# Kernel tuning notes

Measured on AMD Instinct MI355X. Metric: run time of the kernel, lower is better.

## Reference

```python
import jax, jax.numpy as jnp
import numpy as np

N_NODES = 10000
N_EDGES = 160000
D = 512            # input_dim = hidden_size = output_dim
NUM_EXPERTS = 4
N_LAYERS = 2


def setup_inputs() -> dict:
    key = jax.random.key(0)
    k = jax.random.split(key, 7)
    x = jax.random.normal(k[0], (N_NODES, D), dtype=jnp.float32)
    edge_index = jax.random.randint(k[1], (2, N_EDGES), 0, N_NODES, dtype=jnp.int32)
    # Gating network (Linear D -> NUM_EXPERTS)
    gate_w = jax.random.normal(k[2], (D, NUM_EXPERTS), dtype=jnp.float32) * 0.05
    gate_b = jnp.zeros((NUM_EXPERTS,), dtype=jnp.float32)
    # Per-expert SAGEConv weights: lin_r (self/root) and lin_l (neighbor) + bias
    w_self = jax.random.normal(k[3], (NUM_EXPERTS, N_LAYERS, D, D), dtype=jnp.float32) * 0.05
    w_neigh = jax.random.normal(k[4], (NUM_EXPERTS, N_LAYERS, D, D), dtype=jnp.float32) * 0.05
    b_exp = jnp.zeros((NUM_EXPERTS, N_LAYERS, D), dtype=jnp.float32)
    return {"x": x, "edge_index": edge_index, "gate_w": gate_w, "gate_b": gate_b,
            "w_self": w_self, "w_neigh": w_neigh, "b_exp": b_exp, "top_k": 1}


def reference(x, edge_index, gate_w, gate_b, w_self, w_neigh, b_exp, top_k):
    n = x.shape[0]
    src, dst = edge_index[0], edge_index[1]
    # mean-aggregation normalization (PyG SAGEConv aggr='mean'); 0 for isolated nodes
    deg = jax.ops.segment_sum(jnp.ones_like(src, dtype=x.dtype), dst, num_segments=n)
    inv_deg = jnp.where(deg > 0, 1.0 / jnp.maximum(deg, 1.0), 0.0)[:, None]  # [N,1]

    # gating: softmax(Linear(x)) then top-k routing
    gate = jax.nn.softmax(x @ gate_w + gate_b, axis=-1)          # [N, E]
    top_vals, top_idx = jax.lax.top_k(gate, top_k)               # [N, k]

    def expert(ws, wn, b):  # ws, wn: [L, D, D]; b: [L, D]
        h = x
        for l in range(N_LAYERS):
            agg = jax.ops.segment_sum(h[src], dst, num_segments=n) * inv_deg
            # SAGEConv: lin_l(mean_neigh) + lin_r(x) + bias, then relu (norm='id', eval dropout)
            h = jax.nn.relu(agg @ wn[l] + h @ ws[l] + b[l])
        return h

    # dense all-expert compute (matches original module)
    outs = jax.vmap(expert)(w_self, w_neigh, b_exp)              # [E, N, D]
    outs = jnp.transpose(outs, (1, 0, 2))                        # [N, E, D]
    sel = jnp.take_along_axis(outs, top_idx[:, :, None], axis=1)  # [N, k, D]
    return jnp.sum(sel * top_vals[:, :, None], axis=1)           # [N, D]
```

## Files before the change

kernel.cpp:

```cpp
#include <hip/hip_runtime.h>
#include <hip/hip_bf16.h>
#include <cstdint>

#define N_NODES 10000
#define N_EDGES 160000
#define DIM 512
#define K1 1024
#define NEXP 4

typedef __bf16 bf16_t;
typedef bf16_t bf16x8 __attribute__((ext_vector_type(8)));
typedef float f32x4 __attribute__((ext_vector_type(4)));

#define AS1(p) ((__attribute__((address_space(1))) void*)(p))
#define AS3(p) ((__attribute__((address_space(3))) void*)(p))

__global__ void zero_kernel(int* __restrict__ deg, int* __restrict__ ecnt) {
    int i = blockIdx.x * blockDim.x + threadIdx.x;
    if (i < N_NODES) deg[i] = 0;
    if (i < NEXP) ecnt[i] = 0;
}

__global__ void gate_kernel(const float* __restrict__ x,
                            const float* __restrict__ gw,
                            const float* __restrict__ gb,
                            int* __restrict__ top_idx,
                            float* __restrict__ top_val,
                            bf16_t* __restrict__ acat) {
    const int wave = threadIdx.x >> 6;
    const int lane = threadIdx.x & 63;
    const int node = blockIdx.x * 4 + wave;
    if (node >= N_NODES) return;
    const float4* x4 = (const float4*)(x + (size_t)node * DIM);
    const float4* gw4 = (const float4*)gw;
    float4 xa = x4[lane * 2];
    float4 xb = x4[lane * 2 + 1];
    float xv[8] = { xa.x, xa.y, xa.z, xa.w, xb.x, xb.y, xb.z, xb.w };
    float a0 = 0.f, a1 = 0.f, a2 = 0.f, a3 = 0.f;
    #pragma unroll
    for (int c = 0; c < 8; c++) {
        float4 g = gw4[lane * 8 + c];
        a0 += xv[c] * g.x; a1 += xv[c] * g.y; a2 += xv[c] * g.z; a3 += xv[c] * g.w;
    }
    bf16x8 o;
    #pragma unroll
    for (int c = 0; c < 8; c++) o[c] = (bf16_t)xv[c];
    *(bf16x8*)(acat + (size_t)node * K1 + DIM + lane * 8) = o;
    for (int off = 32; off > 0; off >>= 1) {
        a0 += __shfl_xor(a0, off);
        a1 += __shfl_xor(a1, off);
        a2 += __shfl_xor(a2, off);
        a3 += __shfl_xor(a3, off);
    }
    if (lane == 0) {
        float z[4] = { a0 + gb[0], a1 + gb[1], a2 + gb[2], a3 + gb[3] };
        int bi = 0; float bm = z[0];
        for (int e = 1; e < 4; e++) if (z[e] > bm) { bm = z[e]; bi = e; }
        float den = 0.f;
        for (int e = 0; e < 4; e++) den += expf(z[e] - bm);
        top_idx[node] = bi;
        top_val[node] = 1.0f / den;
    }
}

__global__ void bucket_kernel(const int* __restrict__ top_idx,
                              int* __restrict__ ecnt,
                              int* __restrict__ lists) {
    __shared__ int lcnt[NEXP];
    __shared__ int base[NEXP];
    const int tid = threadIdx.x;
    if (tid < NEXP) lcnt[tid] = 0;
    __syncthreads();
    const int node = blockIdx.x * 256 + tid;
    int e = 0, rank = 0;
    if (node < N_NODES) {
        e = top_idx[node];
        rank = atomicAdd(&lcnt[e], 1);
    }
    __syncthreads();
    if (tid < NEXP) base[tid] = atomicAdd(&ecnt[tid], lcnt[tid]);
    __syncthreads();
    if (node < N_NODES) lists[e * N_NODES + base[e] + rank] = node;
}

__global__ void deg_kernel(const int* __restrict__ dst, int* __restrict__ deg) {
    int i = blockIdx.x * blockDim.x + threadIdx.x;
    if (i < N_EDGES) atomicAdd(&deg[dst[i]], 1);
}

__global__ void scan_kernel(const int* __restrict__ deg,
                            int* __restrict__ offs,
                            int* __restrict__ cursor) {
    __shared__ int wsum[16];
    __shared__ int carrysh;
    const int tid = threadIdx.x;
    const int lane = tid & 63;
    const int wv = tid >> 6;
    if (tid == 0) carrysh = 0;
    __syncthreads();
    for (int base = 0; base < N_NODES; base += 1024) {
        int i = base + tid;
        int v = (i < N_NODES) ? deg[i] : 0;
        int s = v;
        #pragma unroll
        for (int off = 1; off < 64; off <<= 1) {
            int t = __shfl_up(s, off);
            if (lane >= off) s += t;
        }
        if (lane == 63) wsum[wv] = s;
        int carry = carrysh;
        __syncthreads();
        if (wv == 0) {
            int w = (lane < 16) ? wsum[lane] : 0;
            #pragma unroll
            for (int off = 1; off < 16; off <<= 1) {
                int t = __shfl_up(w, off);
                if (lane >= off) w += t;
            }
            if (lane < 16) wsum[lane] = w;
        }
        __syncthreads();
        int wbase = (wv > 0) ? wsum[wv - 1] : 0;
        int excl = carry + wbase + s - v;
        if (i < N_NODES) { offs[i] = excl; cursor[i] = excl; }
        int total = wsum[15];
        __syncthreads();
        if (tid == 0) carrysh = carry + total;
        __syncthreads();
    }
    if (tid == 0) offs[N_NODES] = carrysh;
}

__global__ void fill_kernel(const int* __restrict__ src, const int* __restrict__ dst,
                            int* __restrict__ cursor, int* __restrict__ csr) {
    int i = blockIdx.x * blockDim.x + threadIdx.x;
    if (i < N_EDGES) {
        int d = dst[i];
        int p = atomicAdd(&cursor[d], 1);
        csr[p] = src[i];
    }
}

__global__ void wtrans_kernel(const float* __restrict__ w_neigh,
                              const float* __restrict__ w_self,
                              bf16_t* __restrict__ Bt) {
    __shared__ float tile[32][33];
    const int m = blockIdx.z;
    const bool isSelf = m >= 8;
    const int el = m & 7;
    const float* W = (isSelf ? w_self : w_neigh) + (size_t)el * DIM * DIM;
    const int k0 = blockIdx.x * 32;
    const int n0 = blockIdx.y * 32;
    const int tx = threadIdx.x, ty = threadIdx.y;
    for (int r = ty; r < 32; r += 8)
        tile[r][tx] = W[(size_t)(k0 + r) * DIM + n0 + tx];
    __syncthreads();
    for (int r = ty; r < 32; r += 8) {
        int n = n0 + r;
        int k = k0 + tx;
        Bt[((size_t)el * DIM + n) * K1 + (isSelf ? DIM : 0) + k] = (bf16_t)tile[tx][r];
    }
}

__global__ void agg1_kernel(const int* __restrict__ offs, const int* __restrict__ csr,
                            bf16_t* __restrict__ acat) {
    const int wave = threadIdx.x >> 6;
    const int lane = threadIdx.x & 63;
    const int node = blockIdx.x * 4 + wave;
    if (node >= N_NODES) return;
    const int c0 = lane * 8;
    float s[8] = {0,0,0,0,0,0,0,0};
    int beg = offs[node];
    int end = offs[node + 1];
    int d = end - beg;
    int p = beg;
    for (; p + 8 <= end; p += 8) {
        bf16x8 v[8];
        #pragma unroll
        for (int q = 0; q < 8; q++) {
            int idx = csr[p + q];
            v[q] = *(const bf16x8*)(acat + (size_t)idx * K1 + DIM + c0);
        }
        #pragma unroll
        for (int q = 0; q < 8; q++)
            #pragma unroll
            for (int k = 0; k < 8; k++) s[k] += (float)v[q][k];
    }
    for (; p + 4 <= end; p += 4) {
        bf16x8 v[4];
        #pragma unroll
        for (int q = 0; q < 4; q++) {
            int idx = csr[p + q];
            v[q] = *(const bf16x8*)(acat + (size_t)idx * K1 + DIM + c0);
        }
        #pragma unroll
        for (int q = 0; q < 4; q++)
            #pragma unroll
            for (int k = 0; k < 8; k++) s[k] += (float)v[q][k];
    }
    for (; p < end; p++) {
        int idx = csr[p];
        bf16x8 v0 = *(const bf16x8*)(acat + (size_t)idx * K1 + DIM + c0);
        #pragma unroll
        for (int k = 0; k < 8; k++) s[k] += (float)v0[k];
    }
    float w = d > 0 ? 1.0f / (float)d : 0.0f;
    bf16x8 o;
    #pragma unroll
    for (int k = 0; k < 8; k++) o[k] = (bf16_t)(s[k] * w);
    *(bf16x8*)(acat + (size_t)node * K1 + c0) = o;
}

__global__ void agg2_kernel(const int* __restrict__ offs, const int* __restrict__ csr,
                            const int* __restrict__ top_idx,
                            const bf16_t* __restrict__ h1, bf16_t* __restrict__ acat) {
    const int wave = threadIdx.x >> 6;
    const int lane = threadIdx.x & 63;
    const int node = blockIdx.x * 4 + wave;
    if (node >= N_NODES) return;
    const int c0 = lane * 8;
    const bf16_t* hb = h1 + (size_t)top_idx[node] * N_NODES * DIM;
    float s[8] = {0,0,0,0,0,0,0,0};
    int beg = offs[node];
    int end = offs[node + 1];
    int d = end - beg;
    int p = beg;
    for (; p + 8 <= end; p += 8) {
        bf16x8 v[8];
        #pragma unroll
        for (int q = 0; q < 8; q++) {
            int idx = csr[p + q];
            v[q] = *(const bf16x8*)(hb + (size_t)idx * DIM + c0);
        }
        #pragma unroll
        for (int q = 0; q < 8; q++)
            #pragma unroll
            for (int k = 0; k < 8; k++) s[k] += (float)v[q][k];
    }
    for (; p + 4 <= end; p += 4) {
        bf16x8 v[4];
        #pragma unroll
        for (int q = 0; q < 4; q++) {
            int idx = csr[p + q];
            v[q] = *(const bf16x8*)(hb + (size_t)idx * DIM + c0);
        }
        #pragma unroll
        for (int q = 0; q < 4; q++)
            #pragma unroll
            for (int k = 0; k < 8; k++) s[k] += (float)v[q][k];
    }
    for (; p < end; p++) {
        int idx = csr[p];
        bf16x8 v0 = *(const bf16x8*)(hb + (size_t)idx * DIM + c0);
        #pragma unroll
        for (int k = 0; k < 8; k++) s[k] += (float)v0[k];
    }
    float w = d > 0 ? 1.0f / (float)d : 0.0f;
    bf16x8 o;
    #pragma unroll
    for (int k = 0; k < 8; k++) o[k] = (bf16_t)(s[k] * w);
    *(bf16x8*)(acat + (size_t)node * K1 + c0) = o;
    *(bf16x8*)(acat + (size_t)node * K1 + DIM + c0) = *(const bf16x8*)(hb + (size_t)node * DIM + c0);
}

__global__ __launch_bounds__(256)
void gemm1_kernel(const bf16_t* __restrict__ A,
                  const bf16_t* __restrict__ Bt,
                  const float* __restrict__ bias_all,
                  bf16_t* __restrict__ h1) {
    const int b = blockIdx.x;
    const int kq = b & 7;
    const int ke = kq >> 2;
    const int ky = kq & 3;
    const int r = b >> 3;
    const int yloc = r >> 3;
    const int xz = r & 7;
    const int bx = xz & 3;
    const int e = ke * 2 + (xz >> 2);
    const int by = ky * 20 + yloc;
    if (by >= 79) return;

    __shared__ __align__(16) bf16_t As[128 * 32];
    __shared__ __align__(16) bf16_t Bs[128 * 32];

    const int t = threadIdx.x;
    const int lane = t & 63;
    const int wave = t >> 6;
    const int wm = wave >> 1;
    const int wn = wave & 1;

    const int r0 = t >> 2;
    const int rot = (t >> 3) & 3;
    const int cgl = ((t & 3) - rot) & 3;

    int i0 = by * 128 + r0;
    int i1 = i0 + 64;
    int arow0 = min(i0, N_NODES - 1);
    int arow1 = min(i1, N_NODES - 1);

    const bf16_t* Bte = Bt + (size_t)(e * 2) * DIM * K1;
    const bf16_t* aptr0 = A + (size_t)arow0 * K1 + cgl * 8;
    const bf16_t* aptr1 = A + (size_t)arow1 * K1 + cgl * 8;
    const bf16_t* bptr0 = Bte + (size_t)(bx * 128 + r0) * K1 + cgl * 8;
    const bf16_t* bptr1 = bptr0 + (size_t)64 * K1;

    f32x4 acc[4][4] = {};
    char* asb = (char*)&As[0];
    char* bsb = (char*)&Bs[0];
    const int wb = wave * 1024;

    const int cpr = lane >> 4;
    const int rfr = lane & 15;

    for (int k0 = 0; k0 < K1; k0 += 32) {
        __syncthreads();
        __builtin_amdgcn_global_load_lds(AS1(aptr0), AS3(asb + wb),        16, 0, 0);
        __builtin_amdgcn_global_load_lds(AS1(aptr1), AS3(asb + 4096 + wb), 16, 0, 0);
        __builtin_amdgcn_global_load_lds(AS1(bptr0), AS3(bsb + wb),        16, 0, 0);
        __builtin_amdgcn_global_load_lds(AS1(bptr1), AS3(bsb + 4096 + wb), 16, 0, 0);
        __syncthreads();
        bf16x8 af[4], bfr[4];
        #pragma unroll
        for (int i = 0; i < 4; i++) {
            int rf = wm * 64 + i * 16 + rfr;
            int pp = (cpr + (rf >> 1)) & 3;
            af[i] = *(const bf16x8*)(As + rf * 32 + pp * 8);
        }
        #pragma unroll
        for (int j = 0; j < 4; j++) {
            int rf = wn * 64 + j * 16 + rfr;
            int pp = (cpr + (rf >> 1)) & 3;
            bfr[j] = *(const bf16x8*)(Bs + rf * 32 + pp * 8);
        }
        #pragma unroll
        for (int i = 0; i < 4; i++)
            #pragma unroll
            for (int j = 0; j < 4; j++)
                acc[i][j] = __builtin_amdgcn_mfma_f32_16x16x32_bf16(af[i], bfr[j], acc[i][j], 0, 0, 0);
        aptr0 += 32; aptr1 += 32; bptr0 += 32; bptr1 += 32;
    }

    const float* bias = bias_all + e * 1024;
    const int cbase = bx * 128 + wn * 64 + (lane & 15);
    float bv[4];
    #pragma unroll
    for (int j = 0; j < 4; j++) bv[j] = bias[cbase + j * 16];
    #pragma unroll
    for (int i = 0; i < 4; i++) {
        #pragma unroll
        for (int rr = 0; rr < 4; rr++) {
            int row = by * 128 + wm * 64 + i * 16 + (lane >> 4) * 4 + rr;
            if (row < N_NODES) {
                bf16_t* cp = h1 + ((size_t)e * N_NODES + row) * DIM + cbase;
                #pragma unroll
                for (int j = 0; j < 4; j++) {
                    float v = fmaxf(acc[i][j][rr] + bv[j], 0.f);
                    cp[j * 16] = (bf16_t)v;
                }
            }
        }
    }
}

__global__ __launch_bounds__(256)
void gemm2_kernel(const bf16_t* __restrict__ A,
                  const bf16_t* __restrict__ Bt,
                  const float* __restrict__ bias_all,
                  float* __restrict__ out,
                  const int* __restrict__ lists,
                  const int* __restrict__ ecnt,
                  const float* __restrict__ top_val) {
    const int bx = blockIdx.x, by = blockIdx.y, e = blockIdx.z;
    const int cnt = ecnt[e];
    if (by * 64 >= cnt) return;

    __shared__ __align__(16) bf16_t As[64 * 32];
    __shared__ __align__(16) bf16_t Bs[128 * 32];

    const int t = threadIdx.x;
    const int lane = t & 63;
    const int wave = t >> 6;

    const int r0 = t >> 2;
    const int rot = (t >> 3) & 3;
    const int cgl = ((t & 3) - rot) & 3;

    int i0 = by * 64 + r0;
    int arow0 = lists[e * N_NODES + min(i0, cnt - 1)];

    const bf16_t* Bte = Bt + (size_t)(e * 2 + 1) * DIM * K1;
    const bf16_t* aptr0 = A + (size_t)arow0 * K1 + cgl * 8;
    const bf16_t* bptr0 = Bte + (size_t)(bx * 128 + r0) * K1 + cgl * 8;
    const bf16_t* bptr1 = bptr0 + (size_t)64 * K1;

    f32x4 acc[4][2] = {};
    char* asb = (char*)&As[0];
    char* bsb = (char*)&Bs[0];
    const int wb = wave * 1024;

    const int cpr = lane >> 4;
    const int rfr = lane & 15;

    for (int k0 = 0; k0 < K1; k0 += 32) {
        __syncthreads();
        __builtin_amdgcn_global_load_lds(AS1(aptr0), AS3(asb + wb),        16, 0, 0);
        __builtin_amdgcn_global_load_lds(AS1(bptr0), AS3(bsb + wb),        16, 0, 0);
        __builtin_amdgcn_global_load_lds(AS1(bptr1), AS3(bsb + 4096 + wb), 16, 0, 0);
        __syncthreads();
        bf16x8 af[4], bfr[2];
        #pragma unroll
        for (int i = 0; i < 4; i++) {
            int rf = i * 16 + rfr;
            int pp = (cpr + (rf >> 1)) & 3;
            af[i] = *(const bf16x8*)(As + rf * 32 + pp * 8);
        }
        #pragma unroll
        for (int j = 0; j < 2; j++) {
            int rf = wave * 32 + j * 16 + rfr;
            int pp = (cpr + (rf >> 1)) & 3;
            bfr[j] = *(const bf16x8*)(Bs + rf * 32 + pp * 8);
        }
        #pragma unroll
        for (int i = 0; i < 4; i++)
            #pragma unroll
            for (int j = 0; j < 2; j++)
                acc[i][j] = __builtin_amdgcn_mfma_f32_16x16x32_bf16(af[i], bfr[j], acc[i][j], 0, 0, 0);
        aptr0 += 32; bptr0 += 32; bptr1 += 32;
    }

    const float* bias = bias_all + e * 1024 + DIM;
    const int cbase = bx * 128 + wave * 32 + (lane & 15);
    float bv[2];
    #pragma unroll
    for (int j = 0; j < 2; j++) bv[j] = bias[cbase + j * 16];
    #pragma unroll
    for (int i = 0; i < 4; i++) {
        #pragma unroll
        for (int rr = 0; rr < 4; rr++) {
            int row = by * 64 + i * 16 + (lane >> 4) * 4 + rr;
            if (row < cnt) {
                int node = lists[e * N_NODES + row];
                float tv = top_val[node];
                float* cp = out + (size_t)node * DIM + cbase;
                #pragma unroll
                for (int j = 0; j < 2; j++) {
                    float v = fmaxf(acc[i][j][rr] + bv[j], 0.f);
                    cp[j * 16] = v * tv;
                }
            }
        }
    }
}

extern "C" void kernel_launch(void* const* d_in, const int* in_sizes, int n_in,
                              void* d_out, int out_size, void* d_ws, size_t ws_size,
                              hipStream_t stream) {
    const float* x       = (const float*)d_in[0];
    const int*   edge    = (const int*)d_in[1];
    const float* gw      = (const float*)d_in[2];
    const float* gb      = (const float*)d_in[3];
    const float* w_self  = (const float*)d_in[4];
    const float* w_neigh = (const float*)d_in[5];
    const float* b_exp   = (const float*)d_in[6];
    float* out = (float*)d_out;

    char* p = (char*)d_ws;
    auto alloc = [&](size_t bytes) {
        char* r = p;
        p += (bytes + 255) & ~(size_t)255;
        return r;
    };
    bf16_t* Bt      = (bf16_t*)alloc((size_t)8 * DIM * K1 * 2);
    bf16_t* acat    = (bf16_t*)alloc((size_t)N_NODES * K1 * 2);
    bf16_t* h1      = (bf16_t*)alloc((size_t)NEXP * N_NODES * DIM * 2);
    int*    deg     = (int*)alloc((size_t)N_NODES * 4);
    int*    offs    = (int*)alloc((size_t)(N_NODES + 1) * 4);
    int*    cursor  = (int*)alloc((size_t)N_NODES * 4);
    int*    csr     = (int*)alloc((size_t)N_EDGES * 4);
    int*    top_idx = (int*)alloc((size_t)N_NODES * 4);
    float*  top_val = (float*)alloc((size_t)N_NODES * 4);
    int*    ecnt    = (int*)alloc(256);
    int*    lists   = (int*)alloc((size_t)NEXP * N_NODES * 4);

    const int* srcE = edge;
    const int* dstE = edge + N_EDGES;

    zero_kernel<<<40, 256, 0, stream>>>(deg, ecnt);
    gate_kernel<<<N_NODES / 4, 256, 0, stream>>>(x, gw, gb, top_idx, top_val, acat);
    bucket_kernel<<<40, 256, 0, stream>>>(top_idx, ecnt, lists);
    deg_kernel<<<N_EDGES / 256, 256, 0, stream>>>(dstE, deg);
    scan_kernel<<<1, 1024, 0, stream>>>(deg, offs, cursor);
    fill_kernel<<<N_EDGES / 256, 256, 0, stream>>>(srcE, dstE, cursor, csr);
    wtrans_kernel<<<dim3(16, 16, 16), dim3(32, 8), 0, stream>>>(w_neigh, w_self, Bt);
    agg1_kernel<<<N_NODES / 4, 256, 0, stream>>>(offs, csr, acat);
    gemm1_kernel<<<1280, 256, 0, stream>>>(acat, Bt, b_exp, h1);
    agg2_kernel<<<N_NODES / 4, 256, 0, stream>>>(offs, csr, top_idx, h1, acat);
    gemm2_kernel<<<dim3(4, 157, 4), 256, 0, stream>>>(acat, Bt, b_exp, out, lists, ecnt, top_val);
}
```

Before: 281.2 us.

## Double-buffer LDS tiles in both GEMM kernels to overlap loads with MFMA

Both GEMM kernels now keep two LDS buffers for the A and B tiles. The next K-slice is issued with global_load_lds before the MFMAs on the current slice, and each iteration needs one barrier instead of two. The goal is to hide global-to-LDS latency behind matrix compute and cut barrier stalls. In exchange it doubles shared memory per block, which can lower occupancy, and it relies on the barrier also waiting for the outstanding async loads.

```diff
diff --git a/kernel.cpp b/kernel.cpp
--- a/kernel.cpp
+++ b/kernel.cpp
@@ -280,8 +280,8 @@
     const int by = ky * 20 + yloc;
     if (by >= 79) return;
 
-    __shared__ __align__(16) bf16_t As[128 * 32];
-    __shared__ __align__(16) bf16_t Bs[128 * 32];
+    __shared__ __align__(16) bf16_t As[2][128 * 32];
+    __shared__ __align__(16) bf16_t Bs[2][128 * 32];
 
     const int t = threadIdx.x;
     const int lane = t & 63;
@@ -305,39 +305,51 @@
     const bf16_t* bptr1 = bptr0 + (size_t)64 * K1;
 
     f32x4 acc[4][4] = {};
-    char* asb = (char*)&As[0];
-    char* bsb = (char*)&Bs[0];
+    char* asb = (char*)&As[0][0];
+    char* bsb = (char*)&Bs[0][0];
     const int wb = wave * 1024;
 
     const int cpr = lane >> 4;
     const int rfr = lane & 15;
 
+    __builtin_amdgcn_global_load_lds(AS1(aptr0), AS3(asb + wb),        16, 0, 0);
+    __builtin_amdgcn_global_load_lds(AS1(aptr1), AS3(asb + 4096 + wb), 16, 0, 0);
+    __builtin_amdgcn_global_load_lds(AS1(bptr0), AS3(bsb + wb),        16, 0, 0);
+    __builtin_amdgcn_global_load_lds(AS1(bptr1), AS3(bsb + 4096 + wb), 16, 0, 0);
+    aptr0 += 32; aptr1 += 32; bptr0 += 32; bptr1 += 32;
+    __syncthreads();
+
     for (int k0 = 0; k0 < K1; k0 += 32) {
-        __syncthreads();
-        __builtin_amdgcn_global_load_lds(AS1(aptr0), AS3(asb + wb),        16, 0, 0);
-        __builtin_amdgcn_global_load_lds(AS1(aptr1), AS3(asb + 4096 + wb), 16, 0, 0);
-        __builtin_amdgcn_global_load_lds(AS1(bptr0), AS3(bsb + wb),        16, 0, 0);
-        __builtin_amdgcn_global_load_lds(AS1(bptr1), AS3(bsb + 4096 + wb), 16, 0, 0);
-        __syncthreads();
+        const int cur = (k0 >> 5) & 1;
+        const int nb = (cur ^ 1) * 8192;
+        if (k0 + 32 < K1) {
+            __builtin_amdgcn_global_load_lds(AS1(aptr0), AS3(asb + nb + wb),        16, 0, 0);
+            __builtin_amdgcn_global_load_lds(AS1(aptr1), AS3(asb + nb + 4096 + wb), 16, 0, 0);
+            __builtin_amdgcn_global_load_lds(AS1(bptr0), AS3(bsb + nb + wb),        16, 0, 0);
+            __builtin_amdgcn_global_load_lds(AS1(bptr1), AS3(bsb + nb + 4096 + wb), 16, 0, 0);
+            aptr0 += 32; aptr1 += 32; bptr0 += 32; bptr1 += 32;
+        }
+        const bf16_t* Ac = &As[cur][0];
+        const bf16_t* Bc = &Bs[cur][0];
         bf16x8 af[4], bfr[4];
         #pragma unroll
         for (int i = 0; i < 4; i++) {
             int rf = wm * 64 + i * 16 + rfr;
             int pp = (cpr + (rf >> 1)) & 3;
-            af[i] = *(const bf16x8*)(As + rf * 32 + pp * 8);
+            af[i] = *(const bf16x8*)(Ac + rf * 32 + pp * 8);
         }
         #pragma unroll
         for (int j = 0; j < 4; j++) {
             int rf = wn * 64 + j * 16 + rfr;
             int pp = (cpr + (rf >> 1)) & 3;
-            bfr[j] = *(const bf16x8*)(Bs + rf * 32 + pp * 8);
+            bfr[j] = *(const bf16x8*)(Bc + rf * 32 + pp * 8);
         }
         #pragma unroll
         for (int i = 0; i < 4; i++)
             #pragma unroll
             for (int j = 0; j < 4; j++)
                 acc[i][j] = __builtin_amdgcn_mfma_f32_16x16x32_bf16(af[i], bfr[j], acc[i][j], 0, 0, 0);
-        aptr0 += 32; aptr1 += 32; bptr0 += 32; bptr1 += 32;
+        __syncthreads();
     }
 
     const float* bias = bias_all + e * 1024;
@@ -374,8 +386,8 @@
     const int cnt = ecnt[e];
     if (by * 64 >= cnt) return;
 
-    __shared__ __align__(16) bf16_t As[64 * 32];
-    __shared__ __align__(16) bf16_t Bs[128 * 32];
+    __shared__ __align__(16) bf16_t As[2][64 * 32];
+    __shared__ __align__(16) bf16_t Bs[2][128 * 32];
 
     const int t = threadIdx.x;
     const int lane = t & 63;
@@ -394,38 +406,50 @@
     const bf16_t* bptr1 = bptr0 + (size_t)64 * K1;
 
     f32x4 acc[4][2] = {};
-    char* asb = (char*)&As[0];
-    char* bsb = (char*)&Bs[0];
+    char* asb = (char*)&As[0][0];
+    char* bsb = (char*)&Bs[0][0];
     const int wb = wave * 1024;
 
     const int cpr = lane >> 4;
     const int rfr = lane & 15;
 
+    __builtin_amdgcn_global_load_lds(AS1(aptr0), AS3(asb + wb),        16, 0, 0);
+    __builtin_amdgcn_global_load_lds(AS1(bptr0), AS3(bsb + wb),        16, 0, 0);
+    __builtin_amdgcn_global_load_lds(AS1(bptr1), AS3(bsb + 4096 + wb), 16, 0, 0);
+    aptr0 += 32; bptr0 += 32; bptr1 += 32;
+    __syncthreads();
+
     for (int k0 = 0; k0 < K1; k0 += 32) {
-        __syncthreads();
-        __builtin_amdgcn_global_load_lds(AS1(aptr0), AS3(asb + wb),        16, 0, 0);
-        __builtin_amdgcn_global_load_lds(AS1(bptr0), AS3(bsb + wb),        16, 0, 0);
-        __builtin_amdgcn_global_load_lds(AS1(bptr1), AS3(bsb + 4096 + wb), 16, 0, 0);
-        __syncthreads();
+        const int cur = (k0 >> 5) & 1;
+        if (k0 + 32 < K1) {
+            const int na = (cur ^ 1) * 4096;
+            const int nb = (cur ^ 1) * 8192;
+            __builtin_amdgcn_global_load_lds(AS1(aptr0), AS3(asb + na + wb),        16, 0, 0);
+            __builtin_amdgcn_global_load_lds(AS1(bptr0), AS3(bsb + nb + wb),        16, 0, 0);
+            __builtin_amdgcn_global_load_lds(AS1(bptr1), AS3(bsb + nb + 4096 + wb), 16, 0, 0);
+            aptr0 += 32; bptr0 += 32; bptr1 += 32;
+        }
+        const bf16_t* Ac = &As[cur][0];
+        const bf16_t* Bc = &Bs[cur][0];
         bf16x8 af[4], bfr[2];
         #pragma unroll
         for (int i = 0; i < 4; i++) {
             int rf = i * 16 + rfr;
             int pp = (cpr + (rf >> 1)) & 3;
-            af[i] = *(const bf16x8*)(As + rf * 32 + pp * 8);
+            af[i] = *(const bf16x8*)(Ac + rf * 32 + pp * 8);
         }
         #pragma unroll
         for (int j = 0; j < 2; j++) {
             int rf = wave * 32 + j * 16 + rfr;
             int pp = (cpr + (rf >> 1)) & 3;
-            bfr[j] = *(const bf16x8*)(Bs + rf * 32 + pp * 8);
+            bfr[j] = *(const bf16x8*)(Bc + rf * 32 + pp * 8);
         }
         #pragma unroll
         for (int i = 0; i < 4; i++)
             #pragma unroll
             for (int j = 0; j < 2; j++)
                 acc[i][j] = __builtin_amdgcn_mfma_f32_16x16x32_bf16(af[i], bfr[j], acc[i][j], 0, 0, 0);
-        aptr0 += 32; bptr0 += 32; bptr1 += 32;
+        __syncthreads();
     }
 
     const float* bias = bias_all + e * 1024 + DIM;
```

Measured after the change: 282.9 us. No clear change (+0.6%).
